# Kernel optimization log

Hardware: AMD Instinct MI355X
Metric: run time of the kernel (lower is better)

## Reference

```python
import jax, jax.numpy as jnp
import numpy as np

B, S, IN, D, HID, H, K, YD = 4, 2048, 64, 128, 400, 4, 20, 4
WHICH_OUT = 0
ALPHAS = jnp.array([0.05, 0.06, 0.08, 0.1, 0.12, 0.14, 0.15, 0.17, 0.19, 0.2,
                    0.21, 0.23, 0.25, 0.3, 0.35, 0.38, 0.4, 0.45], dtype=jnp.float32)  # 18 alphas


def _mlp(x, W1, b1, W2, b2, W3, b3, W4, b4):
    # FcModel encoder: in -> 400 -> 400 -> 400 -> out, ReLU hidden, linear head
    h = jax.nn.relu(x @ W1 + b1)
    h = jax.nn.relu(h @ W2 + b2)
    h = jax.nn.relu(h @ W3 + b3)
    return h @ W4 + b4


def _ln(x, g, b):
    mu = jnp.mean(x, axis=-1, keepdims=True)
    var = jnp.var(x, axis=-1, keepdims=True)
    return (x - mu) * jax.lax.rsqrt(var + 1e-5) * g + b


def setup_inputs() -> dict:
    key = jax.random.key(0)
    ks = jax.random.split(key, 16)
    w = lambda k, shape: 0.05 * jax.random.normal(k, shape, dtype=jnp.float32)
    return {
        'X_ctx_true': jax.random.normal(ks[0], (B, S, IN), dtype=jnp.float32),
        'X_ctx_sim':  jax.random.normal(ks[1], (B, S, IN), dtype=jnp.float32),
        'errors':     jax.random.normal(ks[2], (B, S, YD), dtype=jnp.float32),
        'y':          jax.random.normal(ks[3], (B, S, YD), dtype=jnp.float32),
        'y_pred':     jax.random.normal(ks[4], (B, S, YD), dtype=jnp.float32),
        'W1': w(ks[5], (IN, HID)),  'b1': jnp.zeros((HID,), jnp.float32),
        'W2': w(ks[6], (HID, HID)), 'b2': jnp.zeros((HID,), jnp.float32),
        'W3': w(ks[7], (HID, HID)), 'b3': jnp.zeros((HID,), jnp.float32),
        'W4': w(ks[8], (HID, D)),   'b4': jnp.zeros((D,), jnp.float32),
        'Wq': w(ks[9], (D, H * D)), 'bq': jnp.zeros((H * D,), jnp.float32),
        'Wk': w(ks[10], (D, H * D)), 'bk': jnp.zeros((H * D,), jnp.float32),
        'g_q': jnp.ones((D,), jnp.float32), 'beta_q': jnp.zeros((D,), jnp.float32),
        'g_k': jnp.ones((D,), jnp.float32), 'beta_k': jnp.zeros((D,), jnp.float32),
    }


def reference(X_ctx_true, X_ctx_sim, errors, y, y_pred,
              W1, b1, W2, b2, W3, b3, W4, b4,
              Wq, bq, Wk, bk, g_q, beta_q, g_k, beta_k):
    err_w = errors[..., WHICH_OUT]                      # [B,S]
    enc_true = _mlp(X_ctx_true, W1, b1, W2, b2, W3, b3, W4, b4)  # [B,S,D]
    enc_sim = _mlp(X_ctx_sim, W1, b1, W2, b2, W3, b3, W4, b4)    # [B,S,D]

    # Hopfield association: LayerNorm on state (query) and stored (key) patterns,
    # per-head projection to hidden_size=D, scaled dot product, diag mask, softmax.
    q = (_ln(enc_true, g_q, beta_q) @ Wq + bq).reshape(B, S, H, D)
    k = (_ln(enc_sim, g_k, beta_k) @ Wk + bk).reshape(B, S, H, D)
    scores = jnp.einsum('bshd,bmhd->bhsm', q, k) / jnp.sqrt(jnp.float32(D))
    diag = jnp.eye(S, dtype=bool)
    scores = jnp.where(diag[None, None], -jnp.inf, scores)
    assoc = jax.nn.softmax(scores, axis=-1)             # [B,H,S,M]

    # topk sampling of memory slots, gather corresponding errors
    _, idx = jax.lax.top_k(assoc, K)                    # [B,H,S,K]
    sel = err_w[jnp.arange(B)[:, None, None, None], idx]  # [B,H,S,K]

    # quantiles over samples for all alphas at once (torch.quantile = linear interp)
    betas = ALPHAS / 2.0
    q_low = jnp.quantile(sel, betas, axis=-1)           # [A,B,H,S]
    q_high = jnp.quantile(sel, 1.0 - ALPHAS + betas, axis=-1)  # [A,B,H,S]

    yp = y_pred[..., WHICH_OUT]                         # [B,S]
    y_low = q_low + yp[None, :, None, :]                # [A,B,H,S]
    y_high = q_high + yp[None, :, None, :]

    # mean-quantile MSE score, per head then averaged
    mean_err = jnp.concatenate([q_low, q_high], axis=0).mean(axis=0)  # [B,H,S]
    pred_adj = mean_err + yp[:, None, :]                # [B,H,S]
    y_true = y[..., WHICH_OUT]                          # [B,S]
    scores_per_head = jnp.mean((y_true[:, None, :] - pred_adj) ** 2, axis=(0, 2))  # [H]
    score = jnp.mean(scores_per_head)

    to_out = lambda a: jnp.transpose(a, (2, 1, 0, 3))[..., None]  # [A,B,H,S]->[H,B,A,S,1]
    return (score, y, y_pred, to_out(y_low), to_out(y_high),
            errors[..., WHICH_OUT:WHICH_OUT + 1], to_out(q_low), to_out(q_high))
```

## Files before the change

kernel.cpp:

```cpp
#include <hip/hip_runtime.h>
#include <hip/hip_bf16.h>
#include <math.h>


#define SS 2048

typedef short short8v __attribute__((ext_vector_type(8)));
typedef float float4v __attribute__((ext_vector_type(4)));
typedef float float2v __attribute__((ext_vector_type(2)));

__constant__ float c_alphas[18] = {0.05f,0.06f,0.08f,0.1f,0.12f,0.14f,0.15f,0.17f,
                                   0.19f,0.2f,0.21f,0.23f,0.25f,0.3f,0.35f,0.38f,0.4f,0.45f};

#define OFF_Y      1
#define OFF_YPRED  32769
#define OFF_YLOW   65537ll
#define OFF_YHIGH  655361ll
#define OFF_ERR    1245185ll
#define OFF_QLOW   1253377ll
#define OFF_QHIGH  1843201ll

__device__ inline short f2bf_s(float f) {
    __hip_bfloat16 h = __float2bfloat16(f);
    return __builtin_bit_cast(short, h);
}
__device__ inline unsigned mono(float f) {
    unsigned u = __builtin_bit_cast(unsigned, f);
    return (u & 0x80000000u) ? ~u : (u | 0x80000000u);
}
__device__ inline float rdlane(float v, int l) {
    return __builtin_bit_cast(float, __builtin_amdgcn_readlane(__builtin_bit_cast(int, v), l));
}
__device__ inline unsigned umin_(unsigned a, unsigned b) { return a < b ? a : b; }
__device__ inline unsigned umax_(unsigned a, unsigned b) { return a > b ? a : b; }
__device__ inline float2v pkfma(float x, float2v w, float2v a) {
    return __builtin_elementwise_fma((float2v){x, x}, w, a);
}

__global__ __launch_bounds__(64, 1) void k_mlp(
    const float* __restrict__ Xt, const float* __restrict__ Xs,
    const float* __restrict__ W1, const float* __restrict__ b1,
    const float* __restrict__ W2, const float* __restrict__ b2,
    const float* __restrict__ W3, const float* __restrict__ b3,
    const float* __restrict__ W4, const float* __restrict__ b4,
    const float* __restrict__ Wq, const float* __restrict__ bq,
    const float* __restrict__ Wk, const float* __restrict__ bk,
    const float* __restrict__ g_q, const float* __restrict__ beta_q,
    const float* __restrict__ g_k, const float* __restrict__ beta_k,
    float* __restrict__ qf, float* __restrict__ kf,
    __hip_bfloat16* __restrict__ khi)
{
    const int t    = threadIdx.x;
    const int bi   = blockIdx.x;
    const int half = bi >> 10;
    const int rbase = (bi & 1023) * 8;
    const float* X = half ? Xs : Xt;

    int jm[8];
    #pragma unroll
    for (int cc = 0; cc < 8; ++cc) { int j = cc*64 + t; jm[cc] = (j < 400) ? j : 399; }

    float xreg[8];
    #pragma unroll
    for (int r = 0; r < 8; ++r) xreg[r] = X[(size_t)(rbase + r)*64 + t];

    float2v A1[8][4], A2[8][4];

    {
        #pragma unroll
        for (int r = 0; r < 8; ++r)
            #pragma unroll
            for (int p = 0; p < 4; ++p) A1[r][p] = (float2v){0.f, 0.f};
        #pragma unroll 4
        for (int il = 0; il < 64; ++il) {
            float2v wv[4];
            #pragma unroll
            for (int p = 0; p < 4; ++p)
                wv[p] = (float2v){W1[il*400 + jm[2*p]], W1[il*400 + jm[2*p+1]]};
            #pragma unroll
            for (int r = 0; r < 8; ++r) {
                const float x = rdlane(xreg[r], il);
                #pragma unroll
                for (int p = 0; p < 4; ++p) A1[r][p] = pkfma(x, wv[p], A1[r][p]);
            }
        }
        #pragma unroll
        for (int p = 0; p < 4; ++p) {
            const float2v bb = (float2v){b1[jm[2*p]], b1[jm[2*p+1]]};
            #pragma unroll
            for (int r = 0; r < 8; ++r)
                A1[r][p] = __builtin_elementwise_max(A1[r][p] + bb, (float2v){0.f, 0.f});
        }
    }

    {
        #pragma unroll
        for (int r = 0; r < 8; ++r)
            #pragma unroll
            for (int p = 0; p < 4; ++p) A2[r][p] = (float2v){0.f, 0.f};
        #pragma unroll
        for (int cs = 0; cs < 7; ++cs) {
            const int ilim = (cs == 6) ? 16 : 64;
            #pragma unroll 4
            for (int il = 0; il < ilim; ++il) {
                const int i = cs*64 + il;
                float2v wv[4];
                #pragma unroll
                for (int p = 0; p < 4; ++p)
                    wv[p] = (float2v){W2[i*400 + jm[2*p]], W2[i*400 + jm[2*p+1]]};
                #pragma unroll
                for (int r = 0; r < 8; ++r) {
                    const float x = rdlane(A1[r][cs >> 1][cs & 1], il);
                    #pragma unroll
                    for (int p = 0; p < 4; ++p) A2[r][p] = pkfma(x, wv[p], A2[r][p]);
                }
            }
        }
        #pragma unroll
        for (int p = 0; p < 4; ++p) {
            const float2v bb = (float2v){b2[jm[2*p]], b2[jm[2*p+1]]};
            #pragma unroll
            for (int r = 0; r < 8; ++r)
                A2[r][p] = __builtin_elementwise_max(A2[r][p] + bb, (float2v){0.f, 0.f});
        }
    }

    {
        #pragma unroll
        for (int r = 0; r < 8; ++r)
            #pragma unroll
            for (int p = 0; p < 4; ++p) A1[r][p] = (float2v){0.f, 0.f};
        #pragma unroll
        for (int cs = 0; cs < 7; ++cs) {
            const int ilim = (cs == 6) ? 16 : 64;
            #pragma unroll 4
            for (int il = 0; il < ilim; ++il) {
                const int i = cs*64 + il;
                float2v wv[4];
                #pragma unroll
                for (int p = 0; p < 4; ++p)
                    wv[p] = (float2v){W3[i*400 + jm[2*p]], W3[i*400 + jm[2*p+1]]};
                #pragma unroll
                for (int r = 0; r < 8; ++r) {
                    const float x = rdlane(A2[r][cs >> 1][cs & 1], il);
                    #pragma unroll
                    for (int p = 0; p < 4; ++p) A1[r][p] = pkfma(x, wv[p], A1[r][p]);
                }
            }
        }
        #pragma unroll
        for (int p = 0; p < 4; ++p) {
            const float2v bb = (float2v){b3[jm[2*p]], b3[jm[2*p+1]]};
            #pragma unroll
            for (int r = 0; r < 8; ++r)
                A1[r][p] = __builtin_elementwise_max(A1[r][p] + bb, (float2v){0.f, 0.f});
        }
    }

    float2v acc4[8];
    {
        #pragma unroll
        for (int r = 0; r < 8; ++r) acc4[r] = (float2v){0.f, 0.f};
        #pragma unroll
        for (int cs = 0; cs < 7; ++cs) {
            const int ilim = (cs == 6) ? 16 : 64;
            #pragma unroll 4
            for (int il = 0; il < ilim; ++il) {
                const int i = cs*64 + il;
                const float2v wv = (float2v){W4[i*128 + t], W4[i*128 + 64 + t]};
                #pragma unroll
                for (int r = 0; r < 8; ++r) {
                    const float x = rdlane(A1[r][cs >> 1][cs & 1], il);
                    acc4[r] = pkfma(x, wv, acc4[r]);
                }
            }
        }
        const float2v bb = (float2v){b4[t], b4[64 + t]};
        #pragma unroll
        for (int r = 0; r < 8; ++r) acc4[r] = acc4[r] + bb;
    }

    float2v lnv[8];
    {
        const float* g  = half ? g_k : g_q;
        const float* be = half ? beta_k : beta_q;
        const float gl0 = g[t],  gl1 = g[64 + t];
        const float bl0 = be[t], bl1 = be[64 + t];
        #pragma unroll
        for (int r = 0; r < 8; ++r) {
            float s = acc4[r][0] + acc4[r][1];
            #pragma unroll
            for (int o = 32; o > 0; o >>= 1) s += __shfl_xor(s, o);
            const float mu = s * (1.f/128.f);
            const float d0 = acc4[r][0] - mu, d1 = acc4[r][1] - mu;
            float vs = d0*d0 + d1*d1;
            #pragma unroll
            for (int o = 32; o > 0; o >>= 1) vs += __shfl_xor(vs, o);
            const float rstd = rsqrtf(vs * (1.f/128.f) + 1e-5f);
            lnv[r][0] = d0*rstd*gl0 + bl0;
            lnv[r][1] = d1*rstd*gl1 + bl1;
        }
    }

    {
        const float* Wp = half ? Wk : Wq;
        const float* bp = half ? bk : bq;
        float* of = half ? kf : qf;
        float2v accp[8][4];
        #pragma unroll
        for (int r = 0; r < 8; ++r)
            #pragma unroll
            for (int p = 0; p < 4; ++p) accp[r][p] = (float2v){0.f, 0.f};
        #pragma unroll
        for (int cs = 0; cs < 2; ++cs) {
            #pragma unroll 4
            for (int il = 0; il < 64; ++il) {
                const int i = cs*64 + il;
                float2v wv[4];
                #pragma unroll
                for (int p = 0; p < 4; ++p)
                    wv[p] = (float2v){Wp[i*512 + (2*p)*64 + t], Wp[i*512 + (2*p+1)*64 + t]};
                #pragma unroll
                for (int r = 0; r < 8; ++r) {
                    const float x = rdlane(lnv[r][cs], il);
                    #pragma unroll
                    for (int p = 0; p < 4; ++p) accp[r][p] = pkfma(x, wv[p], accp[r][p]);
                }
            }
        }
        float bpv[8];
        #pragma unroll
        for (int cc = 0; cc < 8; ++cc) bpv[cc] = bp[cc*64 + t];
        #pragma unroll
        for (int r = 0; r < 8; ++r) {
            const int gidx = rbase + r;
            const int bb = gidx >> 11, s = gidx & 2047;
            const int T = s >> 4, m16s = s & 15;
            #pragma unroll
            for (int cc = 0; cc < 8; ++cc) {
                const int j  = cc*64 + t;
                const int hh = j >> 7, d = j & 127;
                const float v = accp[r][cc >> 1][cc & 1] + bpv[cc];
                const size_t dst = ((size_t)(bb*4 + hh)*2048 + s)*128 + d;
                of[dst] = v;
                if (half) {
                    const int ks = d >> 5, qd = (d & 31) >> 3, jj = d & 7;
                    const size_t so = (size_t)(bb*4 + hh)*262144
                                    + (size_t)T*2048 + ks*512 + qd*128 + m16s*8 + jj;
                    khi[so] = __float2bfloat16(v);
                }
            }
        }
    }
}

__global__ __launch_bounds__(256, 4) void k_scan(
    const float* __restrict__ qf, const __hip_bfloat16* __restrict__ khi,
    unsigned* __restrict__ wsk)
{
    __shared__ unsigned kd[64*97];

    const int tid   = threadIdx.x;
    const int stile = blockIdx.x;
    const int hb    = blockIdx.y;
    const int mq    = blockIdx.z;

    const int lane = tid & 63;
    const int w    = tid >> 6;
    const int m16  = lane & 15;
    const int quad = lane >> 4;

    const size_t slab = (size_t)hb * 2048;
    const __hip_bfloat16* slabp = khi + (size_t)hb * 262144;

    const int sg_my = stile*64 + w*16 + m16;

    short8v bq_[4];
    {
        const float* qp = qf + (slab + sg_my)*128 + quad*8;
        #pragma unroll
        for (int ks = 0; ks < 4; ++ks) {
            const float4 x0 = *(const float4*)(qp + ks*32);
            const float4 x1 = *(const float4*)(qp + ks*32 + 4);
            short8v tt;
            tt[0]=f2bf_s(x0.x); tt[1]=f2bf_s(x0.y); tt[2]=f2bf_s(x0.z); tt[3]=f2bf_s(x0.w);
            tt[4]=f2bf_s(x1.x); tt[5]=f2bf_s(x1.y); tt[6]=f2bf_s(x1.z); tt[7]=f2bf_s(x1.w);
            bq_[ks] = tt;
        }
    }

    unsigned KA[12], KB[12];
    #pragma unroll
    for (int n = 0; n < 12; ++n) { KA[n] = 0u; KB[n] = 0u; }

    #pragma unroll 1
    for (int cti = 0; cti < 32; ++cti) {
        const int T = mq*32 + cti;
        const __hip_bfloat16* kp = slabp + (size_t)T*2048 + lane*8;
        float4v acc = (float4v){0.f,0.f,0.f,0.f};
        #pragma unroll
        for (int ks = 0; ks < 4; ++ks) {
            const short8v ka = *(const short8v*)(kp + ks*512);
            acc = __builtin_amdgcn_mfma_f32_16x16x32_bf16(ka, bq_[ks], acc, 0, 0, 0);
        }
        const int cb = T*16 + quad*4;
        #pragma unroll
        for (int ph = 0; ph < 2; ++ph) {
            {
                const int m = cb + ph;
                unsigned key = (mono(acc[ph]) & 0xFFFFF800u) | (unsigned)m;
                key = (m == sg_my) ? 0u : key;
                KA[0] = umax_(KA[0], key);
                #pragma unroll
                for (int i = 0; i < 11; ++i) {
                    const unsigned a = KA[i], c = KA[i+1];
                    KA[i]   = umin_(a, c);
                    KA[i+1] = umax_(a, c);
                }
            }
            {
                const int m = cb + 2 + ph;
                unsigned key = (mono(acc[2+ph]) & 0xFFFFF800u) | (unsigned)m;
                key = (m == sg_my) ? 0u : key;
                KB[0] = umax_(KB[0], key);
                #pragma unroll
                for (int i = 0; i < 11; ++i) {
                    const unsigned a = KB[i], c = KB[i+1];
                    KB[i]   = umin_(a, c);
                    KB[i+1] = umax_(a, c);
                }
            }
        }
    }

    const int rr = w*16 + m16;
    #pragma unroll
    for (int n = 0; n < 12; ++n) {
        kd[rr*97 + (quad*2 + 0)*12 + n] = KA[11 - n];
        kd[rr*97 + (quad*2 + 1)*12 + n] = KB[11 - n];
    }
    __syncthreads();

    if (quad == 0) {
        const unsigned* R = &kd[rr*97];
        int q0=0,q1=0,q2=0,q3=0,q4=0,q5=0,q6=0,q7=0;
        const size_t base = (size_t)hb*2048 + stile*64 + rr;
        #pragma unroll 1
        for (int n = 0; n < 24; ++n) {
            const unsigned h0 = (q0<12)?R[  0+q0]:0u;
            const unsigned h1 = (q1<12)?R[ 12+q1]:0u;
            const unsigned h2 = (q2<12)?R[ 24+q2]:0u;
            const unsigned h3 = (q3<12)?R[ 36+q3]:0u;
            const unsigned h4 = (q4<12)?R[ 48+q4]:0u;
            const unsigned h5 = (q5<12)?R[ 60+q5]:0u;
            const unsigned h6 = (q6<12)?R[ 72+q6]:0u;
            const unsigned h7 = (q7<12)?R[ 84+q7]:0u;
            unsigned bv = h0; int bs = 0;
            if (h1 > bv) { bv = h1; bs = 1; }
            if (h2 > bv) { bv = h2; bs = 2; }
            if (h3 > bv) { bv = h3; bs = 3; }
            if (h4 > bv) { bv = h4; bs = 4; }
            if (h5 > bv) { bv = h5; bs = 5; }
            if (h6 > bv) { bv = h6; bs = 6; }
            if (h7 > bv) { bv = h7; bs = 7; }
            q0 += (bs==0); q1 += (bs==1); q2 += (bs==2); q3 += (bs==3);
            q4 += (bs==4); q5 += (bs==5); q6 += (bs==6); q7 += (bs==7);
            wsk[(size_t)(mq*24 + n)*32768 + base] = bv;
        }
    }
}

__global__ __launch_bounds__(256, 4) void k_select(
    const float* __restrict__ qf, const float* __restrict__ kf,
    const unsigned* __restrict__ wsk,
    const float* __restrict__ errors, const float* __restrict__ y,
    const float* __restrict__ y_pred,
    float* __restrict__ out, float* __restrict__ hacc)
{
    __shared__ unsigned kd[64*4*25];
    __shared__ unsigned short cb[64*33];
    __shared__ float es[64*33];
    __shared__ float ebuf[64*21];

    const int tid   = threadIdx.x;
    const int stile = blockIdx.x;
    const int hb    = blockIdx.y;
    const int b     = hb >> 2;
    const int h     = hb & 3;

    const int lane = tid & 63;
    const int w    = tid >> 6;
    const int m16  = lane & 15;
    const int quad = lane >> 4;
    const int rr   = w*16 + m16;
    const int sg   = stile*64 + rr;

    const size_t base = (size_t)hb*2048 + sg;
    #pragma unroll 1
    for (int n = 0; n < 24; ++n)
        kd[(rr*4 + quad)*25 + n] = wsk[(size_t)(quad*24 + n)*32768 + base];
    __syncthreads();

    if (quad == 0) {
        const unsigned* L0 = &kd[(rr*4 + 0)*25];
        const unsigned* L1 = &kd[(rr*4 + 1)*25];
        const unsigned* L2 = &kd[(rr*4 + 2)*25];
        const unsigned* L3 = &kd[(rr*4 + 3)*25];
        int p0 = 0, p1 = 0, p2 = 0, p3 = 0;
        #pragma unroll 1
        for (int n = 0; n < 32; ++n) {
            const unsigned h0 = (p0 < 24) ? L0[p0] : 0u;
            const unsigned h1 = (p1 < 24) ? L1[p1] : 0u;
            const unsigned h2 = (p2 < 24) ? L2[p2] : 0u;
            const unsigned h3 = (p3 < 24) ? L3[p3] : 0u;
            unsigned bv = h0; int bs = 0;
            if (h1 > bv) { bv = h1; bs = 1; }
            if (h2 > bv) { bv = h2; bs = 2; }
            if (h3 > bv) { bv = h3; bs = 3; }
            if (bs == 0) ++p0; else if (bs == 1) ++p1; else if (bs == 2) ++p2; else ++p3;
            cb[rr*33 + n] = (unsigned short)(bv & 0x7FFu);
        }
    }
    __syncthreads();

    const size_t slab = (size_t)hb * 2048;
    const float* qrow_p = qf + (slab + sg)*128;
    float4 qseg[8];
    #pragma unroll
    for (int u = 0; u < 8; ++u)
        qseg[u] = *(const float4*)(qrow_p + quad*4 + u*16);
    const float* kslab = kf + slab*128;
    #pragma unroll 1
    for (int n = 0; n < 32; ++n) {
        const int col = cb[rr*33 + n];
        const float* kc = kslab + (size_t)col*128 + quad*4;
        float2v s01 = (float2v){0.f, 0.f}, s23 = (float2v){0.f, 0.f};
        #pragma unroll
        for (int u = 0; u < 8; ++u) {
            const float4 kv = *(const float4*)(kc + u*16);
            s01 = __builtin_elementwise_fma((float2v){qseg[u].x, qseg[u].y},
                                            (float2v){kv.x, kv.y}, s01);
            s23 = __builtin_elementwise_fma((float2v){qseg[u].z, qseg[u].w},
                                            (float2v){kv.z, kv.w}, s23);
        }
        float v = (s01[0] + s01[1]) + (s23[0] + s23[1]);
        v += __shfl_xor(v, 16);
        v += __shfl_xor(v, 32);
        if (quad == 0) es[rr*33 + n] = v;
    }

    float sq = 0.f;
    if (quad == 0) {
        float* e = &ebuf[rr*21];
        #pragma unroll 1
        for (int k = 0; k < 20; ++k) {
            float best = -INFINITY; int bc = 4096, bj = 0;
            #pragma unroll 1
            for (int j = 0; j < 32; ++j) {
                const float v = es[rr*33 + j];
                const int c = cb[rr*33 + j];
                if (v > best || (v == best && c < bc)) { best = v; bc = c; bj = j; }
            }
            es[rr*33 + bj] = -INFINITY;
            e[k] = errors[((size_t)(b*SS + bc))*4];
        }
        #pragma unroll 1
        for (int a = 1; a < 20; ++a) {
            const float v = e[a];
            int n = a;
            while (n > 0 && e[n-1] > v) { e[n] = e[n-1]; --n; }
            e[n] = v;
        }
        const float yp = y_pred[((size_t)(b*SS + sg))*4];
        const float yt = y[((size_t)(b*SS + sg))*4];
        float msum = 0.f;
        const size_t obase = ((size_t)(h*4 + b)*18)*2048 + sg;
        #pragma unroll 1
        for (int a = 0; a < 18; ++a) {
            const float alpha = c_alphas[a];
            const float beta  = 0.5f*alpha;
            const float pl = beta * 19.f;
            const int   il = (int)pl;
            const float fl = pl - (float)il;
            const float ql = e[il]*(1.f-fl) + e[il+1]*fl;
            const float qq = (1.f - alpha) + beta;
            const float ph = qq * 19.f;
            const int   ih = (int)ph;
            const float fh = ph - (float)ih;
            const float qh = e[ih]*(1.f-fh) + e[ih+1]*fh;
            msum += ql + qh;
            const size_t oidx = obase + (size_t)a*2048;
            out[OFF_YLOW  + oidx] = ql + yp;
            out[OFF_YHIGH + oidx] = qh + yp;
            out[OFF_QLOW  + oidx] = ql;
            out[OFF_QHIGH + oidx] = qh;
        }
        const float me = msum * (1.f/36.f);
        const float dd = yt - (me + yp);
        sq = dd*dd;
    }
    #pragma unroll
    for (int o = 32; o > 0; o >>= 1) sq += __shfl_xor(sq, o);
    if (lane == 0) atomicAdd(&hacc[h], sq);
}

__global__ void k_init(float* __restrict__ hacc) {
    if (threadIdx.x < 4) hacc[threadIdx.x] = 0.f;
}

__global__ __launch_bounds__(256) void k_finalize(
    const float* __restrict__ y, const float* __restrict__ y_pred,
    const float* __restrict__ errors, const float* __restrict__ hacc,
    float* __restrict__ out)
{
    const int i = blockIdx.x*256 + threadIdx.x;
    if (i == 0)
        out[0] = (hacc[0]+hacc[1]+hacc[2]+hacc[3]) * (1.f/32768.f);
    if (i < 32768)      out[OFF_Y + i] = y[i];
    else if (i < 65536) out[OFF_YPRED + (i - 32768)] = y_pred[i - 32768];
    else if (i < 73728) { const int j = i - 65536; out[OFF_ERR + j] = errors[(size_t)j*4]; }
}

extern "C" void kernel_launch(void* const* d_in, const int* in_sizes, int n_in,
                              void* d_out, int out_size, void* d_ws, size_t ws_size,
                              hipStream_t stream)
{
    const float* Xt     = (const float*)d_in[0];
    const float* Xs     = (const float*)d_in[1];
    const float* errors = (const float*)d_in[2];
    const float* y      = (const float*)d_in[3];
    const float* y_pred = (const float*)d_in[4];
    const float* W1 = (const float*)d_in[5];   const float* b1 = (const float*)d_in[6];
    const float* W2 = (const float*)d_in[7];   const float* b2 = (const float*)d_in[8];
    const float* W3 = (const float*)d_in[9];   const float* b3 = (const float*)d_in[10];
    const float* W4 = (const float*)d_in[11];  const float* b4 = (const float*)d_in[12];
    const float* Wq = (const float*)d_in[13];  const float* bq = (const float*)d_in[14];
    const float* Wk = (const float*)d_in[15];  const float* bk = (const float*)d_in[16];
    const float* g_q    = (const float*)d_in[17];
    const float* beta_q = (const float*)d_in[18];
    const float* g_k    = (const float*)d_in[19];
    const float* beta_k = (const float*)d_in[20];

    float* out  = (float*)d_out;
    char*  base = (char*)d_ws;
    const size_t SLAB = (size_t)16*2048*128;
    float* hacc = (float*)base;
    float* qf   = (float*)(base + 256);
    float* kf   = qf + SLAB;
    __hip_bfloat16* khi = (__hip_bfloat16*)(kf + SLAB);
    unsigned* wsk = (unsigned*)(khi + SLAB);

    k_init<<<1, 64, 0, stream>>>(hacc);
    k_mlp<<<2048, 64, 0, stream>>>(Xt, Xs, W1,b1,W2,b2,W3,b3,W4,b4,
                                   Wq,bq,Wk,bk,g_q,beta_q,g_k,beta_k,
                                   qf, kf, khi);
    k_scan<<<dim3(32,16,4), 256, 0, stream>>>(qf, khi, wsk);
    k_select<<<dim3(32,16), 256, 0, stream>>>(qf, kf, wsk, errors, y, y_pred, out, hacc);
    k_finalize<<<288, 256, 0, stream>>>(y, y_pred, errors, hacc, out);
}
```

Baseline: 689.2 us.

## Restructure MLP kernel to 4-wave blocks sharing activations through LDS

The fused MLP/projection kernel changes from one 64-thread wave handling 8 rows with all 400 outputs in registers (using readlane broadcasts) to 256-thread blocks handling 16 rows. Activations are staged in shared memory, and each wave computes a 128-column slice of every layer. Inputs come in as float4 LDS reads instead of scalar readlane, and each weight load is reused across twice as many rows. This cuts register pressure and weight traffic per row but adds block barriers between layers and LDS bandwidth demand.

```diff
diff --git a/kernel.cpp b/kernel.cpp
--- a/kernel.cpp
+++ b/kernel.cpp
@@ -4,6 +4,8 @@
 
 
 #define SS 2048
+#define ROWS 16
+#define AST 400
 
 typedef short short8v __attribute__((ext_vector_type(8)));
 typedef float float4v __attribute__((ext_vector_type(4)));
@@ -28,16 +30,63 @@
     unsigned u = __builtin_bit_cast(unsigned, f);
     return (u & 0x80000000u) ? ~u : (u | 0x80000000u);
 }
-__device__ inline float rdlane(float v, int l) {
-    return __builtin_bit_cast(float, __builtin_amdgcn_readlane(__builtin_bit_cast(int, v), l));
-}
 __device__ inline unsigned umin_(unsigned a, unsigned b) { return a < b ? a : b; }
 __device__ inline unsigned umax_(unsigned a, unsigned b) { return a > b ? a : b; }
-__device__ inline float2v pkfma(float x, float2v w, float2v a) {
-    return __builtin_elementwise_fma((float2v){x, x}, w, a);
-}
-
-__global__ __launch_bounds__(64, 1) void k_mlp(
+
+
+template<int IN_W, int NCC>
+__device__ __forceinline__ void mlp_layer_acc(
+    const float* __restrict__ W, const float* __restrict__ act,
+    const int w, const int t, float (&acc)[ROWS][2])
+{
+    int jm[2];
+    #pragma unroll
+    for (int cc = 0; cc < NCC; ++cc) {
+        const int j = w*128 + cc*64 + t;
+        jm[cc] = (j < 400) ? j : 399;
+    }
+    #pragma unroll
+    for (int r = 0; r < ROWS; ++r)
+        #pragma unroll
+        for (int cc = 0; cc < NCC; ++cc) acc[r][cc] = 0.f;
+
+    #pragma unroll 2
+    for (int i4 = 0; i4 < IN_W/4; ++i4) {
+        float wv[4][2];
+        #pragma unroll
+        for (int jj = 0; jj < 4; ++jj)
+            #pragma unroll
+            for (int cc = 0; cc < NCC; ++cc)
+                wv[jj][cc] = W[(i4*4 + jj)*400 + jm[cc]];
+        #pragma unroll
+        for (int r = 0; r < ROWS; ++r) {
+            const float4v xv = *(const float4v*)(act + r*AST + i4*4);
+            #pragma unroll
+            for (int jj = 0; jj < 4; ++jj)
+                #pragma unroll
+                for (int cc = 0; cc < NCC; ++cc)
+                    acc[r][cc] = fmaf(xv[jj], wv[jj][cc], acc[r][cc]);
+        }
+    }
+}
+
+__device__ __forceinline__ void mlp_layer_store(
+    const float* __restrict__ b, float* __restrict__ act,
+    const int w, const int t, const int ncc, const float (&acc)[ROWS][2])
+{
+    #pragma unroll
+    for (int cc = 0; cc < 2; ++cc) {
+        const int j = w*128 + cc*64 + t;
+        if (cc < ncc && j < 400) {
+            const float bv = b[j];
+            #pragma unroll
+            for (int r = 0; r < ROWS; ++r)
+                act[r*AST + j] = fmaxf(acc[r][cc] + bv, 0.f);
+        }
+    }
+}
+
+__global__ __launch_bounds__(256, 4) void k_mlp(
     const float* __restrict__ Xt, const float* __restrict__ Xs,
     const float* __restrict__ W1, const float* __restrict__ b1,
     const float* __restrict__ W2, const float* __restrict__ b2,
@@ -50,197 +99,134 @@
     float* __restrict__ qf, float* __restrict__ kf,
     __hip_bfloat16* __restrict__ khi)
 {
-    const int t    = threadIdx.x;
+    __shared__ float act[ROWS*AST];
+
+    const int tid  = threadIdx.x;
+    const int t    = tid & 63;
+    const int w    = tid >> 6;
     const int bi   = blockIdx.x;
-    const int half = bi >> 10;
-    const int rbase = (bi & 1023) * 8;
+    const int half = bi >> 9;
+    const int rbase = (bi & 511) * ROWS;
     const float* X = half ? Xs : Xt;
 
-    int jm[8];
-    #pragma unroll
-    for (int cc = 0; cc < 8; ++cc) { int j = cc*64 + t; jm[cc] = (j < 400) ? j : 399; }
-
-    float xreg[8];
-    #pragma unroll
-    for (int r = 0; r < 8; ++r) xreg[r] = X[(size_t)(rbase + r)*64 + t];
-
-    float2v A1[8][4], A2[8][4];
-
+    #pragma unroll
+    for (int u = 0; u < (ROWS*64)/256; ++u) {
+        const int e = u*256 + tid;
+        act[(e >> 6)*AST + (e & 63)] = X[(size_t)rbase*64 + e];
+    }
+    __syncthreads();
+
+    float acc[ROWS][2];
+    const int ncc = (w == 3) ? 1 : 2;
+
+    if (w == 3) mlp_layer_acc<64,1>(W1, act, w, t, acc);
+    else        mlp_layer_acc<64,2>(W1, act, w, t, acc);
+    __syncthreads();
+    mlp_layer_store(b1, act, w, t, ncc, acc);
+    __syncthreads();
+
+    if (w == 3) mlp_layer_acc<400,1>(W2, act, w, t, acc);
+    else        mlp_layer_acc<400,2>(W2, act, w, t, acc);
+    __syncthreads();
+    mlp_layer_store(b2, act, w, t, ncc, acc);
+    __syncthreads();
+
+    if (w == 3) mlp_layer_acc<400,1>(W3, act, w, t, acc);
+    else        mlp_layer_acc<400,2>(W3, act, w, t, acc);
+    __syncthreads();
+    mlp_layer_store(b3, act, w, t, ncc, acc);
+    __syncthreads();
+
+    float2v a4[4];
+    #pragma unroll
+    for (int rr = 0; rr < 4; ++rr) a4[rr] = (float2v){0.f, 0.f};
+    #pragma unroll 2
+    for (int i4 = 0; i4 < 100; ++i4) {
+        float wv0[4], wv1[4];
+        #pragma unroll
+        for (int jj = 0; jj < 4; ++jj) {
+            wv0[jj] = W4[(i4*4 + jj)*128 + t];
+            wv1[jj] = W4[(i4*4 + jj)*128 + 64 + t];
+        }
+        #pragma unroll
+        for (int rr = 0; rr < 4; ++rr) {
+            const float4v xv = *(const float4v*)(act + (w*4 + rr)*AST + i4*4);
+            #pragma unroll
+            for (int jj = 0; jj < 4; ++jj) {
+                a4[rr][0] = fmaf(xv[jj], wv0[jj], a4[rr][0]);
+                a4[rr][1] = fmaf(xv[jj], wv1[jj], a4[rr][1]);
+            }
+        }
+    }
     {
-        #pragma unroll
-        for (int r = 0; r < 8; ++r)
-            #pragma unroll
-            for (int p = 0; p < 4; ++p) A1[r][p] = (float2v){0.f, 0.f};
-        #pragma unroll 4
-        for (int il = 0; il < 64; ++il) {
-            float2v wv[4];
-            #pragma unroll
-            for (int p = 0; p < 4; ++p)
-                wv[p] = (float2v){W1[il*400 + jm[2*p]], W1[il*400 + jm[2*p+1]]};
-            #pragma unroll
-            for (int r = 0; r < 8; ++r) {
-                const float x = rdlane(xreg[r], il);
-                #pragma unroll
-                for (int p = 0; p < 4; ++p) A1[r][p] = pkfma(x, wv[p], A1[r][p]);
-            }
-        }
-        #pragma unroll
-        for (int p = 0; p < 4; ++p) {
-            const float2v bb = (float2v){b1[jm[2*p]], b1[jm[2*p+1]]};
-            #pragma unroll
-            for (int r = 0; r < 8; ++r)
-                A1[r][p] = __builtin_elementwise_max(A1[r][p] + bb, (float2v){0.f, 0.f});
-        }
-    }
-
-    {
-        #pragma unroll
-        for (int r = 0; r < 8; ++r)
-            #pragma unroll
-            for (int p = 0; p < 4; ++p) A2[r][p] = (float2v){0.f, 0.f};
-        #pragma unroll
-        for (int cs = 0; cs < 7; ++cs) {
-            const int ilim = (cs == 6) ? 16 : 64;
-            #pragma unroll 4
-            for (int il = 0; il < ilim; ++il) {
-                const int i = cs*64 + il;
-                float2v wv[4];
-                #pragma unroll
-                for (int p = 0; p < 4; ++p)
-                    wv[p] = (float2v){W2[i*400 + jm[2*p]], W2[i*400 + jm[2*p+1]]};
-                #pragma unroll
-                for (int r = 0; r < 8; ++r) {
-                    const float x = rdlane(A1[r][cs >> 1][cs & 1], il);
-                    #pragma unroll
-                    for (int p = 0; p < 4; ++p) A2[r][p] = pkfma(x, wv[p], A2[r][p]);
-                }
-            }
-        }
-        #pragma unroll
-        for (int p = 0; p < 4; ++p) {
-            const float2v bb = (float2v){b2[jm[2*p]], b2[jm[2*p+1]]};
-            #pragma unroll
-            for (int r = 0; r < 8; ++r)
-                A2[r][p] = __builtin_elementwise_max(A2[r][p] + bb, (float2v){0.f, 0.f});
-        }
-    }
-
-    {
-        #pragma unroll
-        for (int r = 0; r < 8; ++r)
-            #pragma unroll
-            for (int p = 0; p < 4; ++p) A1[r][p] = (float2v){0.f, 0.f};
-        #pragma unroll
-        for (int cs = 0; cs < 7; ++cs) {
-            const int ilim = (cs == 6) ? 16 : 64;
-            #pragma unroll 4
-            for (int il = 0; il < ilim; ++il) {
-                const int i = cs*64 + il;
-                float2v wv[4];
-                #pragma unroll
-                for (int p = 0; p < 4; ++p)
-                    wv[p] = (float2v){W3[i*400 + jm[2*p]], W3[i*400 + jm[2*p+1]]};
-                #pragma unroll
-                for (int r = 0; r < 8; ++r) {
-                    const float x = rdlane(A2[r][cs >> 1][cs & 1], il);
-                    #pragma unroll
-                    for (int p = 0; p < 4; ++p) A1[r][p] = pkfma(x, wv[p], A1[r][p]);
-                }
-            }
-        }
-        #pragma unroll
-        for (int p = 0; p < 4; ++p) {
-            const float2v bb = (float2v){b3[jm[2*p]], b3[jm[2*p+1]]};
-            #pragma unroll
-            for (int r = 0; r < 8; ++r)
-                A1[r][p] = __builtin_elementwise_max(A1[r][p] + bb, (float2v){0.f, 0.f});
-        }
-    }
-
-    float2v acc4[8];
-    {
-        #pragma unroll
-        for (int r = 0; r < 8; ++r) acc4[r] = (float2v){0.f, 0.f};
-        #pragma unroll
-        for (int cs = 0; cs < 7; ++cs) {
-            const int ilim = (cs == 6) ? 16 : 64;
-            #pragma unroll 4
-            for (int il = 0; il < ilim; ++il) {
-                const int i = cs*64 + il;
-                const float2v wv = (float2v){W4[i*128 + t], W4[i*128 + 64 + t]};
-                #pragma unroll
-                for (int r = 0; r < 8; ++r) {
-                    const float x = rdlane(A1[r][cs >> 1][cs & 1], il);
-                    acc4[r] = pkfma(x, wv, acc4[r]);
-                }
-            }
-        }
-        const float2v bb = (float2v){b4[t], b4[64 + t]};
-        #pragma unroll
-        for (int r = 0; r < 8; ++r) acc4[r] = acc4[r] + bb;
-    }
-
-    float2v lnv[8];
+        const float b40 = b4[t], b41 = b4[64 + t];
+        #pragma unroll
+        for (int rr = 0; rr < 4; ++rr) { a4[rr][0] += b40; a4[rr][1] += b41; }
+    }
+    __syncthreads();
+
     {
         const float* g  = half ? g_k : g_q;
         const float* be = half ? beta_k : beta_q;
         const float gl0 = g[t],  gl1 = g[64 + t];
         const float bl0 = be[t], bl1 = be[64 + t];
         #pragma unroll
-        for (int r = 0; r < 8; ++r) {
-            float s = acc4[r][0] + acc4[r][1];
+        for (int rr = 0; rr < 4; ++rr) {
+            float s = a4[rr][0] + a4[rr][1];
             #pragma unroll
             for (int o = 32; o > 0; o >>= 1) s += __shfl_xor(s, o);
             const float mu = s * (1.f/128.f);
-            const float d0 = acc4[r][0] - mu, d1 = acc4[r][1] - mu;
+            const float d0 = a4[rr][0] - mu, d1 = a4[rr][1] - mu;
             float vs = d0*d0 + d1*d1;
             #pragma unroll
             for (int o = 32; o > 0; o >>= 1) vs += __shfl_xor(vs, o);
             const float rstd = rsqrtf(vs * (1.f/128.f) + 1e-5f);
-            lnv[r][0] = d0*rstd*gl0 + bl0;
-            lnv[r][1] = d1*rstd*gl1 + bl1;
-        }
-    }
+            act[(w*4 + rr)*128 + t]      = d0*rstd*gl0 + bl0;
+            act[(w*4 + rr)*128 + 64 + t] = d1*rstd*gl1 + bl1;
+        }
+    }
+    __syncthreads();
 
     {
         const float* Wp = half ? Wk : Wq;
         const float* bp = half ? bk : bq;
         float* of = half ? kf : qf;
-        float2v accp[8][4];
-        #pragma unroll
-        for (int r = 0; r < 8; ++r)
-            #pragma unroll
-            for (int p = 0; p < 4; ++p) accp[r][p] = (float2v){0.f, 0.f};
-        #pragma unroll
-        for (int cs = 0; cs < 2; ++cs) {
-            #pragma unroll 4
-            for (int il = 0; il < 64; ++il) {
-                const int i = cs*64 + il;
-                float2v wv[4];
+
+        float accp[ROWS][2];
+        #pragma unroll
+        for (int r = 0; r < ROWS; ++r) { accp[r][0] = 0.f; accp[r][1] = 0.f; }
+        #pragma unroll 2
+        for (int i4 = 0; i4 < 32; ++i4) {
+            float wv[4][2];
+            #pragma unroll
+            for (int jj = 0; jj < 4; ++jj)
                 #pragma unroll
-                for (int p = 0; p < 4; ++p)
-                    wv[p] = (float2v){Wp[i*512 + (2*p)*64 + t], Wp[i*512 + (2*p+1)*64 + t]};
+                for (int cc = 0; cc < 2; ++cc)
+                    wv[jj][cc] = Wp[(i4*4 + jj)*512 + w*128 + cc*64 + t];
+            #pragma unroll
+            for (int r = 0; r < ROWS; ++r) {
+                const float4v xv = *(const float4v*)(act + r*128 + i4*4);
                 #pragma unroll
-                for (int r = 0; r < 8; ++r) {
-                    const float x = rdlane(lnv[r][cs], il);
+                for (int jj = 0; jj < 4; ++jj)
                     #pragma unroll
-                    for (int p = 0; p < 4; ++p) accp[r][p] = pkfma(x, wv[p], accp[r][p]);
-                }
+                    for (int cc = 0; cc < 2; ++cc)
+                        accp[r][cc] = fmaf(xv[jj], wv[jj][cc], accp[r][cc]);
             }
         }
-        float bpv[8];
-        #pragma unroll
-        for (int cc = 0; cc < 8; ++cc) bpv[cc] = bp[cc*64 + t];
-        #pragma unroll
-        for (int r = 0; r < 8; ++r) {
+
+        float bpv[2];
+        bpv[0] = bp[w*128 + t];
+        bpv[1] = bp[w*128 + 64 + t];
+        #pragma unroll
+        for (int r = 0; r < ROWS; ++r) {
             const int gidx = rbase + r;
             const int bb = gidx >> 11, s = gidx & 2047;
             const int T = s >> 4, m16s = s & 15;
             #pragma unroll
-            for (int cc = 0; cc < 8; ++cc) {
-                const int j  = cc*64 + t;
+            for (int cc = 0; cc < 2; ++cc) {
+                const int j  = w*128 + cc*64 + t;
                 const int hh = j >> 7, d = j & 127;
-                const float v = accp[r][cc >> 1][cc & 1] + bpv[cc];
+                const float v = accp[r][cc] + bpv[cc];
                 const size_t dst = ((size_t)(bb*4 + hh)*2048 + s)*128 + d;
                 of[dst] = v;
                 if (half) {
@@ -551,9 +537,9 @@
     unsigned* wsk = (unsigned*)(khi + SLAB);
 
     k_init<<<1, 64, 0, stream>>>(hacc);
-    k_mlp<<<2048, 64, 0, stream>>>(Xt, Xs, W1,b1,W2,b2,W3,b3,W4,b4,
-                                   Wq,bq,Wk,bk,g_q,beta_q,g_k,beta_k,
-                                   qf, kf, khi);
+    k_mlp<<<1024, 256, 0, stream>>>(Xt, Xs, W1,b1,W2,b2,W3,b3,W4,b4,
+                                    Wq,bq,Wk,bk,g_q,beta_q,g_k,beta_k,
+                                    qf, kf, khi);
     k_scan<<<dim3(32,16,4), 256, 0, stream>>>(qf, khi, wsk);
     k_select<<<dim3(32,16), 256, 0, stream>>>(qf, kf, wsk, errors, y, y_pred, out, hacc);
     k_finalize<<<288, 256, 0, stream>>>(y, y_pred, errors, hacc, out);
```

New measurement: 610.7 us. 1.13x faster.
